# Performance work log

Hardware: AMD Instinct MI355X
Metric: run time of the kernel (lower is better)

## Reference

```python
import jax, jax.numpy as jnp
import numpy as np

E = 23   # unique experts
K = 3    # active experts per token
D = 1024 # in_features
H = 4096 # hidden_features

def setup_inputs() -> dict:
    key = jax.random.key(0)
    ks = jax.random.split(key, 8)
    s = jnp.float32(0.02)
    return {
        "x": jax.random.normal(ks[0], (4, 2048, D), jnp.float32),
        "gate_W": jax.random.normal(ks[1], (D, E), jnp.float32) * s,
        "gate_b": jnp.zeros((E,), jnp.float32),
        "W1": jax.random.normal(ks[2], (E, D, H), jnp.float32) * s,
        "b1": jnp.zeros((E, H), jnp.float32),
        "W2": jax.random.normal(ks[3], (E, H, D), jnp.float32) * s,
        "b2": jnp.zeros((E, D), jnp.float32),
        "sW1": jax.random.normal(ks[4], (D, H), jnp.float32) * s,
        "sb1": jnp.zeros((H,), jnp.float32),
        "sW2": jax.random.normal(ks[5], (H, D), jnp.float32) * s,
        "sb2": jnp.zeros((D,), jnp.float32),
        "bias": jnp.zeros((E,), jnp.float32),  # registered buffer, zeros
    }

def _mlp(x, w1, bb1, w2, bb2):
    # torch nn.GELU default is exact (erf) GELU; drop=0 so dropout is identity
    return jax.nn.gelu(x @ w1 + bb1, approximate=False) @ w2 + bb2

def reference(x, gate_W, gate_b, W1, b1, W2, b2, sW1, sb1, sW2, sb2, bias):
    oshape = x.shape
    xf = x.reshape(-1, oshape[-1])            # [N, D]
    N = xf.shape[0]
    gw = jax.nn.sigmoid(xf @ gate_W + gate_b) # [N, E]
    # top-k selected on (gate + bias), weights gathered from raw gate
    _, topi = jax.lax.top_k(gw + bias, K)     # [N, K]
    topw = jnp.take_along_axis(gw, topi, axis=-1)
    topw = topw / topw.sum(-1, keepdims=True)
    # dense [N, E] combine-weight matrix (0 for unselected experts);
    # per-token topk indices are distinct so .set is safe
    wmat = jnp.zeros((N, E), gw.dtype).at[jnp.arange(N)[:, None], topi].set(topw)
    shared = _mlp(xf, sW1, sb1, sW2, sb2)     # shared expert over all tokens
    # scan over the 23 experts, accumulating weighted expert outputs.
    # (jit-friendly stand-in for the variable-size dispatch/grouped-GEMM.)
    def body(acc, ws):
        w1, bb1, w2, bb2, wcol = ws
        return acc + wcol[:, None] * _mlp(xf, w1, bb1, w2, bb2), None
    out, _ = jax.lax.scan(body, shared, (W1, b1, W2, b2, wmat.T))
    # load-balance auxiliary loss
    counts = jnp.zeros((E,), jnp.float32).at[topi.reshape(-1)].add(1.0)
    P = (gw / gw.sum(-1, keepdims=True)).mean(0)
    Fload = E * counts / (K * N)
    return out.reshape(oshape), (P * Fload).sum()
```

## Files before the change

kernel.cpp:

```cpp
#include <hip/hip_runtime.h>
#include <math.h>

#define DD 1024
#define HH 4096
#define EE 23
#define KK 3
#define NTOK 8192
#define BM 128
#define BN 128
#define BK 32
#define MAXROWS 35712
#define MAXTILES 280

typedef unsigned short u16;
typedef __attribute__((ext_vector_type(8))) short bf16x8;
typedef __attribute__((ext_vector_type(4))) float f32x4;
typedef __attribute__((address_space(3))) unsigned int lds_u32;
typedef const __attribute__((address_space(1))) unsigned int gbl_u32;

struct Tile { int rowStart; int validEnd; int expert; };

__device__ __forceinline__ u16 f2bf(float f) {
    unsigned int u = __float_as_uint(f);
    unsigned int r = 0x7FFFu + ((u >> 16) & 1u);
    return (u16)((u + r) >> 16);
}
__device__ __forceinline__ float gelu_exact(float x) {
    float z = x * 0.70710678118654752f;
    float a = fabsf(z);
    float t = __builtin_amdgcn_rcpf(1.0f + 0.3275911f * a);
    float e = __builtin_amdgcn_exp2f(-a * a * 1.4426950408889634f);
    float p = t * (0.254829592f + t * (-0.284496736f + t * (1.421413741f +
              t * (-1.453152027f + t * 1.061405429f))));
    float er = 1.0f - p * e;
    er = (z < 0.0f) ? -er : er;
    return 0.5f * x * (1.0f + er);
}
__device__ __forceinline__ void gl2lds16(const u16* g, u16* l) {
    __builtin_amdgcn_global_load_lds((gbl_u32*)g, (lds_u32*)l, 16, 0, 0);
}

__global__ void k_convert_x(const float* __restrict__ x, u16* __restrict__ xbf) {
    int i = blockIdx.x * blockDim.x + threadIdx.x;
    float4 v = reinterpret_cast<const float4*>(x)[i];
    ushort4 o;
    o.x = f2bf(v.x); o.y = f2bf(v.y); o.z = f2bf(v.z); o.w = f2bf(v.w);
    reinterpret_cast<ushort4*>(xbf)[i] = o;
}

__global__ void k_transpose(const float* __restrict__ srcE, u16* __restrict__ dstE,
                            const float* __restrict__ srcS, u16* __restrict__ dstS,
                            int R, int C) {
    __shared__ float tile[64][65];
    const float* src; u16* dst;
    if (blockIdx.z == EE) { src = srcS; dst = dstS; }
    else { size_t base = (size_t)blockIdx.z * R * C; src = srcE + base; dst = dstE + base; }
    int ct = blockIdx.x, rt = blockIdx.y, t = threadIdx.x;
    int r0 = rt * 64, c0 = ct * 64;
#pragma unroll
    for (int i = 0; i < 4; i++) {
        int r = i * 16 + (t >> 4);
        int c = (t & 15) * 4;
        float4 v = *reinterpret_cast<const float4*>(&src[(size_t)(r0 + r) * C + c0 + c]);
        tile[r][c] = v.x; tile[r][c + 1] = v.y; tile[r][c + 2] = v.z; tile[r][c + 3] = v.w;
    }
    __syncthreads();
#pragma unroll
    for (int i = 0; i < 4; i++) {
        int c = i * 16 + (t >> 4);
        int r = (t & 15) * 4;
        ushort4 o;
        o.x = f2bf(tile[r][c]);     o.y = f2bf(tile[r + 1][c]);
        o.z = f2bf(tile[r + 2][c]); o.w = f2bf(tile[r + 3][c]);
        *reinterpret_cast<ushort4*>(&dst[(size_t)(c0 + c) * R + r0 + r]) = o;
    }
}

__global__ void k_gate(const float* __restrict__ x, const float* __restrict__ gW,
                       const float* __restrict__ gb, const float* __restrict__ ebias,
                       int* __restrict__ topi, float* __restrict__ topw,
                       int* __restrict__ counts, float* __restrict__ psum) {
    int tok = blockIdx.x, t = threadIdx.x;
    float acc[EE];
#pragma unroll
    for (int e = 0; e < EE; e++) acc[e] = 0.f;
    float4 xv = reinterpret_cast<const float4*>(x + (size_t)tok * DD)[t];
    float xs[4] = {xv.x, xv.y, xv.z, xv.w};
#pragma unroll
    for (int i = 0; i < 4; i++) {
        const float* grow = gW + (size_t)(t * 4 + i) * EE;
        float xd = xs[i];
#pragma unroll
        for (int e = 0; e < EE; e++) acc[e] += xd * grow[e];
    }
#pragma unroll
    for (int e = 0; e < EE; e++) {
        float v = acc[e];
        for (int off = 32; off; off >>= 1) v += __shfl_down(v, off);
        acc[e] = v;
    }
    __shared__ float part[4][EE];
    __shared__ float gwS[EE], scoreS[EE], rowsumS;
    int wave = t >> 6, lane = t & 63;
    if (lane == 0) {
#pragma unroll
        for (int e = 0; e < EE; e++) part[wave][e] = acc[e];
    }
    __syncthreads();
    if (t < EE) {
        float v = part[0][t] + part[1][t] + part[2][t] + part[3][t] + gb[t];
        float g = 1.f / (1.f + expf(-v));
        gwS[t] = g;
        scoreS[t] = g + ebias[t];
    }
    __syncthreads();
    if (t == 0) {
        int i0 = 0, i1 = -1, i2 = -1;
        float s0 = -1e30f, s1 = -1e30f, s2 = -1e30f;
        for (int e = 0; e < EE; e++) {
            float s = scoreS[e];
            if (s > s0)      { s2 = s1; i2 = i1; s1 = s0; i1 = i0; s0 = s; i0 = e; }
            else if (s > s1) { s2 = s1; i2 = i1; s1 = s;  i1 = e; }
            else if (s > s2) { s2 = s;  i2 = e; }
        }
        float w0 = gwS[i0], w1 = gwS[i1], w2 = gwS[i2];
        float wsum = w0 + w1 + w2;
        topi[tok * 3] = i0; topi[tok * 3 + 1] = i1; topi[tok * 3 + 2] = i2;
        topw[tok * 3] = w0 / wsum; topw[tok * 3 + 1] = w1 / wsum; topw[tok * 3 + 2] = w2 / wsum;
        atomicAdd(&counts[i0], 1); atomicAdd(&counts[i1], 1); atomicAdd(&counts[i2], 1);
        float rs = 0.f;
        for (int e = 0; e < EE; e++) rs += gwS[e];
        rowsumS = rs;
    }
    __syncthreads();
    if (t < EE) atomicAdd(&psum[t], gwS[t] / rowsumS);
}

__global__ void k_setup(const int* __restrict__ counts, const float* __restrict__ psum,
                        int* __restrict__ offs, Tile* __restrict__ tiles,
                        int* __restrict__ numTiles, float* __restrict__ out_aux) {
    if (threadIdx.x != 0 || blockIdx.x != 0) return;
    int nt = 0;
    for (int i = 0; i < NTOK / BM; i++) {
        tiles[nt].rowStart = i * BM; tiles[nt].validEnd = NTOK; tiles[nt].expert = EE; nt++;
    }
    int base = NTOK;
    for (int e = 0; e < EE; e++) {
        offs[e] = base;
        int c = counts[e];
        int ntile = (c + BM - 1) / BM;
        for (int i = 0; i < ntile; i++) {
            tiles[nt].rowStart = base + i * BM; tiles[nt].validEnd = base + c; tiles[nt].expert = e; nt++;
        }
        base += ntile * BM;
    }
    numTiles[0] = nt;
    float aux = 0.f;
    for (int e = 0; e < EE; e++)
        aux += (psum[e] / (float)NTOK) * ((float)EE * (float)counts[e] / ((float)KK * (float)NTOK));
    out_aux[0] = aux;
}

__global__ void k_scatter(const int* __restrict__ topi, const float* __restrict__ topw,
                          const int* __restrict__ offs, int* __restrict__ cursor,
                          int* __restrict__ rowTok, float* __restrict__ rowW) {
    int tok = blockIdx.x * blockDim.x + threadIdx.x;
    if (tok >= NTOK) return;
    rowTok[tok] = tok; rowW[tok] = 1.0f;
    for (int k = 0; k < KK; k++) {
        int e = topi[tok * 3 + k];
        int pos = atomicAdd(&cursor[e], 1);
        int slot = offs[e] + pos;
        rowTok[slot] = tok; rowW[slot] = topw[tok * 3 + k];
    }
}

__global__ __launch_bounds__(256) void k_gemm1(
    const u16* __restrict__ xbf, const u16* __restrict__ w1t, const u16* __restrict__ sw1t,
    const float* __restrict__ b1, const float* __restrict__ sb1,
    const int* __restrict__ rowTok, const Tile* __restrict__ tiles,
    const int* __restrict__ numTiles, u16* __restrict__ hbuf, int chunkBase, int hrows) {
    const int T = MAXTILES * (HH / BN);
    int b = blockIdx.x;
    int key = (b & 7) * (T >> 3) + (b >> 3);
    int sid = key >> 5, wi = key & 31;
    int ti = (sid >> 3) * 8 + (wi >> 2);
    int p  = ((sid & 7) << 2) + (wi & 3);
    if (ti >= numTiles[0]) return;
    Tile tl = tiles[ti];
    if (tl.rowStart < chunkBase || tl.rowStart >= chunkBase + hrows) return;
    int e = tl.expert;
    const u16* wbase = (e == EE) ? sw1t : (w1t + (size_t)e * HH * DD);
    const float* bias = (e == EE) ? sb1 : (b1 + (size_t)e * HH);
    int hbase = p * BN;
    int t = threadIdx.x, lane = t & 63, wv = t >> 6, wr = wv >> 1, wc = wv & 1;

    __shared__ u16 As[2][BM * BK];
    __shared__ u16 Bs[2][BN * BK];

    int rbase = wv * 16 + (lane >> 2);
    int c8 = (lane & 3) * 8;
    int s0 = tl.rowStart + rbase, s1 = s0 + 64;
    int tA0 = (s0 < tl.validEnd) ? rowTok[s0] : 0;
    int tA1 = (s1 < tl.validEnd) ? rowTok[s1] : 0;
    const u16* a0 = xbf + (size_t)tA0 * DD + c8;
    const u16* a1 = xbf + (size_t)tA1 * DD + c8;
    const u16* g0 = wbase + (size_t)(hbase + rbase) * DD + c8;
    const u16* g1 = wbase + (size_t)(hbase + 64 + rbase) * DD + c8;

    f32x4 acc[4][4];
#pragma unroll
    for (int m = 0; m < 4; m++)
#pragma unroll
        for (int n = 0; n < 4; n++) acc[m][n] = (f32x4){0.f, 0.f, 0.f, 0.f};

    auto stage = [&](int buf) {
        u16* lA = &As[buf][t * 8];
        u16* lB = &Bs[buf][t * 8];
        gl2lds16(a0, lA); gl2lds16(a1, lA + 2048);
        gl2lds16(g0, lB); gl2lds16(g1, lB + 2048);
        a0 += BK; a1 += BK; g0 += BK; g1 += BK;
    };
    auto compute = [&](int buf) {
        bf16x8 af[4], bw[4];
        int kc = (lane >> 4) * 8;
#pragma unroll
        for (int m = 0; m < 4; m++)
            af[m] = *reinterpret_cast<const bf16x8*>(&As[buf][(wr * 64 + m * 16 + (lane & 15)) * BK + kc]);
#pragma unroll
        for (int n = 0; n < 4; n++)
            bw[n] = *reinterpret_cast<const bf16x8*>(&Bs[buf][(wc * 64 + n * 16 + (lane & 15)) * BK + kc]);
#pragma unroll
        for (int m = 0; m < 4; m++)
#pragma unroll
            for (int n = 0; n < 4; n++)
                acc[m][n] = __builtin_amdgcn_mfma_f32_16x16x32_bf16(af[m], bw[n], acc[m][n], 0, 0, 0);
    };

    const int NK = DD / BK;
    stage(0);
    for (int kt = 0; kt < NK; kt++) {
        __syncthreads();
        if (kt + 1 < NK) stage((kt + 1) & 1);
        compute(kt & 1);
    }

#pragma unroll
    for (int m = 0; m < 4; m++) {
        int rowl = wr * 64 + m * 16 + (lane >> 4) * 4;
#pragma unroll
        for (int r = 0; r < 4; r++) {
            int slotr = tl.rowStart + rowl + r;
            bool valid = slotr < tl.validEnd;
            size_t hoff = (size_t)(slotr - chunkBase) * HH;
#pragma unroll
            for (int n = 0; n < 4; n++) {
                int col = hbase + wc * 64 + n * 16 + (lane & 15);
                float v = acc[m][n][r] + bias[col];
                hbuf[hoff + col] = valid ? f2bf(gelu_exact(v)) : (u16)0;
            }
        }
    }
}

__global__ __launch_bounds__(256) void k_gemm2(
    const u16* __restrict__ hbuf, const u16* __restrict__ w2t, const u16* __restrict__ sw2t,
    const float* __restrict__ b2, const float* __restrict__ sb2,
    const int* __restrict__ rowTok, const float* __restrict__ rowW,
    const Tile* __restrict__ tiles, const int* __restrict__ numTiles,
    float* __restrict__ out, int chunkBase, int hrows) {
    const int T = MAXTILES * (DD / BN);
    int b = blockIdx.x;
    int key = (b & 7) * (T >> 3) + (b >> 3);
    int sid = key >> 2, wi = key & 3;
    int ti = (sid >> 2) * 2 + (wi >> 1);
    int p  = ((sid & 3) << 1) + (wi & 1);
    if (ti >= numTiles[0]) return;
    Tile tl = tiles[ti];
    if (tl.rowStart < chunkBase || tl.rowStart >= chunkBase + hrows) return;
    int e = tl.expert;
    const u16* wbase = (e == EE) ? sw2t : (w2t + (size_t)e * DD * HH);
    const float* bias = (e == EE) ? sb2 : (b2 + (size_t)e * DD);
    int dbase = p * BN;
    int t = threadIdx.x, lane = t & 63, wv = t >> 6, wr = wv >> 1, wc = wv & 1;

    __shared__ u16 As[2][BM * BK];
    __shared__ u16 Bs[2][BN * BK];

    int rbase = wv * 16 + (lane >> 2);
    int c8 = (lane & 3) * 8;
    const u16* a0 = hbuf + (size_t)(tl.rowStart - chunkBase + rbase) * HH + c8;
    const u16* a1 = hbuf + (size_t)(tl.rowStart - chunkBase + 64 + rbase) * HH + c8;
    const u16* g0 = wbase + (size_t)(dbase + rbase) * HH + c8;
    const u16* g1 = wbase + (size_t)(dbase + 64 + rbase) * HH + c8;

    f32x4 acc[4][4];
#pragma unroll
    for (int m = 0; m < 4; m++)
#pragma unroll
        for (int n = 0; n < 4; n++) acc[m][n] = (f32x4){0.f, 0.f, 0.f, 0.f};

    auto stage = [&](int buf) {
        u16* lA = &As[buf][t * 8];
        u16* lB = &Bs[buf][t * 8];
        gl2lds16(a0, lA); gl2lds16(a1, lA + 2048);
        gl2lds16(g0, lB); gl2lds16(g1, lB + 2048);
        a0 += BK; a1 += BK; g0 += BK; g1 += BK;
    };
    auto compute = [&](int buf) {
        bf16x8 af[4], bw[4];
        int kc = (lane >> 4) * 8;
#pragma unroll
        for (int m = 0; m < 4; m++)
            af[m] = *reinterpret_cast<const bf16x8*>(&As[buf][(wr * 64 + m * 16 + (lane & 15)) * BK + kc]);
#pragma unroll
        for (int n = 0; n < 4; n++)
            bw[n] = *reinterpret_cast<const bf16x8*>(&Bs[buf][(wc * 64 + n * 16 + (lane & 15)) * BK + kc]);
#pragma unroll
        for (int m = 0; m < 4; m++)
#pragma unroll
            for (int n = 0; n < 4; n++)
                acc[m][n] = __builtin_amdgcn_mfma_f32_16x16x32_bf16(af[m], bw[n], acc[m][n], 0, 0, 0);
    };

    const int NK = HH / BK;
    stage(0);
    for (int kt = 0; kt < NK; kt++) {
        __syncthreads();
        if (kt + 1 < NK) stage((kt + 1) & 1);
        compute(kt & 1);
    }

#pragma unroll
    for (int m = 0; m < 4; m++) {
        int rowl = wr * 64 + m * 16 + (lane >> 4) * 4;
#pragma unroll
        for (int r = 0; r < 4; r++) {
            int slotr = tl.rowStart + rowl + r;
            if (slotr < tl.validEnd) {
                int tok2 = rowTok[slotr];
                float wgt = rowW[slotr];
                float* orow = out + (size_t)tok2 * DD;
#pragma unroll
                for (int n = 0; n < 4; n++) {
                    int col = dbase + wc * 64 + n * 16 + (lane & 15);
                    float v = acc[m][n][r] + bias[col];
                    atomicAdd(&orow[col], wgt * v);
                }
            }
        }
    }
}

extern "C" void kernel_launch(void* const* d_in, const int* in_sizes, int n_in,
                              void* d_out, int out_size, void* d_ws, size_t ws_size,
                              hipStream_t stream) {
    const float* x    = (const float*)d_in[0];
    const float* gW   = (const float*)d_in[1];
    const float* gb   = (const float*)d_in[2];
    const float* W1   = (const float*)d_in[3];
    const float* b1   = (const float*)d_in[4];
    const float* W2   = (const float*)d_in[5];
    const float* b2   = (const float*)d_in[6];
    const float* sW1  = (const float*)d_in[7];
    const float* sb1  = (const float*)d_in[8];
    const float* sW2  = (const float*)d_in[9];
    const float* sb2  = (const float*)d_in[10];
    const float* ebias = (const float*)d_in[11];
    float* out = (float*)d_out;

    char* w = (char*)d_ws;
    size_t off = 0;
    auto alloc = [&](size_t bytes) -> void* {
        void* p = w + off;
        off += (bytes + 255) & ~(size_t)255;
        return p;
    };
    u16* xbf   = (u16*)alloc((size_t)NTOK * DD * 2);
    u16* w1t   = (u16*)alloc((size_t)EE * HH * DD * 2);
    u16* w2t   = (u16*)alloc((size_t)EE * DD * HH * 2);
    u16* sw1t  = (u16*)alloc((size_t)HH * DD * 2);
    u16* sw2t  = (u16*)alloc((size_t)DD * HH * 2);
    int* topi  = (int*)alloc((size_t)NTOK * 3 * 4);
    float* topw = (float*)alloc((size_t)NTOK * 3 * 4);
    int* counts = (int*)alloc(128);
    float* psum = (float*)alloc(128);
    int* cursor = (int*)alloc(128);
    int* offs   = (int*)alloc(128);
    int* rowTok = (int*)alloc((size_t)MAXROWS * 4);
    float* rowW = (float*)alloc((size_t)MAXROWS * 4);
    Tile* tiles = (Tile*)alloc((size_t)MAXTILES * sizeof(Tile));
    int* numTiles = (int*)alloc(128);

    size_t fixed = off;
    size_t remain = (ws_size > fixed) ? (ws_size - fixed) : 0;
    long hr = (long)(remain / ((size_t)HH * 2));
    if (hr > MAXROWS) hr = MAXROWS;
    hr &= ~(long)127;
    if (hr < 128) hr = 128;
    int hrows = (int)hr;
    int passes = (MAXROWS + hrows - 1) / hrows;
    u16* hbuf = (u16*)(w + fixed);

    hipMemsetAsync(d_out, 0, (size_t)NTOK * DD * 4, stream);
    hipMemsetAsync(counts, 0, 768, stream);

    k_convert_x<<<NTOK, 256, 0, stream>>>(x, xbf);
    k_transpose<<<dim3(HH / 64, DD / 64, EE + 1), 256, 0, stream>>>(W1, w1t, sW1, sw1t, DD, HH);
    k_transpose<<<dim3(DD / 64, HH / 64, EE + 1), 256, 0, stream>>>(W2, w2t, sW2, sw2t, HH, DD);
    k_gate<<<NTOK, 256, 0, stream>>>(x, gW, gb, ebias, topi, topw, counts, psum);
    k_setup<<<1, 64, 0, stream>>>(counts, psum, offs, tiles, numTiles, out + (size_t)NTOK * DD);
    k_scatter<<<NTOK / 256, 256, 0, stream>>>(topi, topw, offs, cursor, rowTok, rowW);

    for (int p = 0; p < passes; p++) {
        k_gemm1<<<MAXTILES * (HH / BN), 256, 0, stream>>>(
            xbf, w1t, sw1t, b1, sb1, rowTok, tiles, numTiles, hbuf, p * hrows, hrows);
        k_gemm2<<<MAXTILES * (DD / BN), 256, 0, stream>>>(
            hbuf, w2t, sw2t, b2, sb2, rowTok, rowW, tiles, numTiles, out, p * hrows, hrows);
    }
}
```

Baseline: 1.585 ms.

## Replace double-buffered prefetch pipeline with two-tile load-then-compute steps in expert GEMMs

Both expert GEMM kernels drop the stage-next/compute-current double-buffer pipeline. Each iteration now loads two K tiles into both LDS buffers, synchronizes, then runs MFMAs over both tiles. This gives the compiler a larger unrolled compute block per barrier and simpler addressing. The cost is that global-to-LDS load latency is no longer overlapped with MFMA work inside a workgroup.

```diff
diff --git a/kernel.cpp b/kernel.cpp
--- a/kernel.cpp
+++ b/kernel.cpp
@@ -214,35 +214,33 @@
 #pragma unroll
         for (int n = 0; n < 4; n++) acc[m][n] = (f32x4){0.f, 0.f, 0.f, 0.f};
 
-    auto stage = [&](int buf) {
-        u16* lA = &As[buf][t * 8];
-        u16* lB = &Bs[buf][t * 8];
-        gl2lds16(a0, lA); gl2lds16(a1, lA + 2048);
-        gl2lds16(g0, lB); gl2lds16(g1, lB + 2048);
+    for (int kt = 0; kt < DD / (2 * BK); kt++) {
+        __syncthreads();
+        { u16* lA = &As[0][t * 8]; u16* lB = &Bs[0][t * 8];
+          gl2lds16(a0, lA); gl2lds16(a1, lA + 2048);
+          gl2lds16(g0, lB); gl2lds16(g1, lB + 2048); }
         a0 += BK; a1 += BK; g0 += BK; g1 += BK;
-    };
-    auto compute = [&](int buf) {
-        bf16x8 af[4], bw[4];
-        int kc = (lane >> 4) * 8;
-#pragma unroll
-        for (int m = 0; m < 4; m++)
-            af[m] = *reinterpret_cast<const bf16x8*>(&As[buf][(wr * 64 + m * 16 + (lane & 15)) * BK + kc]);
-#pragma unroll
-        for (int n = 0; n < 4; n++)
-            bw[n] = *reinterpret_cast<const bf16x8*>(&Bs[buf][(wc * 64 + n * 16 + (lane & 15)) * BK + kc]);
-#pragma unroll
-        for (int m = 0; m < 4; m++)
+        { u16* lA = &As[1][t * 8]; u16* lB = &Bs[1][t * 8];
+          gl2lds16(a0, lA); gl2lds16(a1, lA + 2048);
+          gl2lds16(g0, lB); gl2lds16(g1, lB + 2048); }
+        a0 += BK; a1 += BK; g0 += BK; g1 += BK;
+        __syncthreads();
+#pragma unroll
+        for (int q = 0; q < 2; q++) {
+            bf16x8 af[4], bw[4];
+            int kc = (lane >> 4) * 8;
+#pragma unroll
+            for (int m = 0; m < 4; m++)
+                af[m] = *reinterpret_cast<const bf16x8*>(&As[q][(wr * 64 + m * 16 + (lane & 15)) * BK + kc]);
 #pragma unroll
             for (int n = 0; n < 4; n++)
-                acc[m][n] = __builtin_amdgcn_mfma_f32_16x16x32_bf16(af[m], bw[n], acc[m][n], 0, 0, 0);
-    };
-
-    const int NK = DD / BK;
-    stage(0);
-    for (int kt = 0; kt < NK; kt++) {
-        __syncthreads();
-        if (kt + 1 < NK) stage((kt + 1) & 1);
-        compute(kt & 1);
+                bw[n] = *reinterpret_cast<const bf16x8*>(&Bs[q][(wc * 64 + n * 16 + (lane & 15)) * BK + kc]);
+#pragma unroll
+            for (int m = 0; m < 4; m++)
+#pragma unroll
+                for (int n = 0; n < 4; n++)
+                    acc[m][n] = __builtin_amdgcn_mfma_f32_16x16x32_bf16(af[m], bw[n], acc[m][n], 0, 0, 0);
+        }
     }
 
 #pragma unroll
@@ -300,35 +298,33 @@
 #pragma unroll
         for (int n = 0; n < 4; n++) acc[m][n] = (f32x4){0.f, 0.f, 0.f, 0.f};
 
-    auto stage = [&](int buf) {
-        u16* lA = &As[buf][t * 8];
-        u16* lB = &Bs[buf][t * 8];
-        gl2lds16(a0, lA); gl2lds16(a1, lA + 2048);
-        gl2lds16(g0, lB); gl2lds16(g1, lB + 2048);
+    for (int kt = 0; kt < HH / (2 * BK); kt++) {
+        __syncthreads();
+        { u16* lA = &As[0][t * 8]; u16* lB = &Bs[0][t * 8];
+          gl2lds16(a0, lA); gl2lds16(a1, lA + 2048);
+          gl2lds16(g0, lB); gl2lds16(g1, lB + 2048); }
         a0 += BK; a1 += BK; g0 += BK; g1 += BK;
-    };
-    auto compute = [&](int buf) {
-        bf16x8 af[4], bw[4];
-        int kc = (lane >> 4) * 8;
-#pragma unroll
-        for (int m = 0; m < 4; m++)
-            af[m] = *reinterpret_cast<const bf16x8*>(&As[buf][(wr * 64 + m * 16 + (lane & 15)) * BK + kc]);
-#pragma unroll
-        for (int n = 0; n < 4; n++)
-            bw[n] = *reinterpret_cast<const bf16x8*>(&Bs[buf][(wc * 64 + n * 16 + (lane & 15)) * BK + kc]);
-#pragma unroll
-        for (int m = 0; m < 4; m++)
+        { u16* lA = &As[1][t * 8]; u16* lB = &Bs[1][t * 8];
+          gl2lds16(a0, lA); gl2lds16(a1, lA + 2048);
+          gl2lds16(g0, lB); gl2lds16(g1, lB + 2048); }
+        a0 += BK; a1 += BK; g0 += BK; g1 += BK;
+        __syncthreads();
+#pragma unroll
+        for (int q = 0; q < 2; q++) {
+            bf16x8 af[4], bw[4];
+            int kc = (lane >> 4) * 8;
+#pragma unroll
+            for (int m = 0; m < 4; m++)
+                af[m] = *reinterpret_cast<const bf16x8*>(&As[q][(wr * 64 + m * 16 + (lane & 15)) * BK + kc]);
 #pragma unroll
             for (int n = 0; n < 4; n++)
-                acc[m][n] = __builtin_amdgcn_mfma_f32_16x16x32_bf16(af[m], bw[n], acc[m][n], 0, 0, 0);
-    };
-
-    const int NK = HH / BK;
-    stage(0);
-    for (int kt = 0; kt < NK; kt++) {
-        __syncthreads();
-        if (kt + 1 < NK) stage((kt + 1) & 1);
-        compute(kt & 1);
+                bw[n] = *reinterpret_cast<const bf16x8*>(&Bs[q][(wc * 64 + n * 16 + (lane & 15)) * BK + kc]);
+#pragma unroll
+            for (int m = 0; m < 4; m++)
+#pragma unroll
+                for (int n = 0; n < 4; n++)
+                    acc[m][n] = __builtin_amdgcn_mfma_f32_16x16x32_bf16(af[m], bw[n], acc[m][n], 0, 0, 0);
+        }
     }
 
 #pragma unroll
```

After: 1.750 ms. +10.4%, slower.
